# Performance work log

Measured on AMD Instinct MI355X. Metric: run time of the kernel, lower is better.

The kernel has to match this reference:

```python
import jax, jax.numpy as jnp
import numpy as np

B, C_IN, L = 256, 4, 2048
HNODE, GLEN = 256, 24
SIGMA_CONV, SIGMA_NEU = 0.1, 0.1
DROPPROB = 0.5


def setup_inputs() -> dict:
    key = jax.random.key(0)
    ks = jax.random.split(key, 7)
    x = jax.random.normal(ks[0], (B, C_IN, L), dtype=jnp.float32)
    wConv = SIGMA_CONV * jax.random.normal(ks[1], (HNODE, C_IN, GLEN), dtype=jnp.float32)
    wRect = -jax.random.normal(ks[2], (HNODE,), dtype=jnp.float32)
    wHidden = 0.3 * jax.random.normal(ks[3], (2 * HNODE, 2 * HNODE), dtype=jnp.float32)
    wHiddenBias = 0.3 * jax.random.normal(ks[4], (2 * HNODE,), dtype=jnp.float32)
    wNeu = SIGMA_NEU * jax.random.normal(ks[5], (2 * HNODE, 1), dtype=jnp.float32)
    wNeuBias = SIGMA_NEU * jax.random.normal(ks[6], (1,), dtype=jnp.float32)
    return {"x": x, "wConv": wConv, "wRect": wRect, "wHidden": wHidden,
            "wHiddenBias": wHiddenBias, "wNeu": wNeu, "wNeuBias": wNeuBias}


def reference(x, wConv, wRect, wHidden, wHiddenBias, wNeu, wNeuBias):
    # conv1d, stride 1, no padding: [B, HNODE, L-GLEN+1]
    conv = jax.lax.conv_general_dilated(
        x, wConv, window_strides=(1,), padding='VALID',
        dimension_numbers=('NCH', 'OIH', 'NCH'))
    rect = jnp.maximum(conv + wRect[None, :, None], 0.0)  # bias + relu-clamp
    maxPool = jnp.max(rect, axis=2)   # [B, HNODE]
    avgPool = jnp.mean(rect, axis=2)  # [B, HNODE]
    pool = jnp.concatenate([maxPool, avgPool], axis=1)  # [B, 2*HNODE]
    hid = jnp.maximum(pool @ wHidden + wHiddenBias, 0.0)
    out = DROPPROB * (hid @ wNeu) + wNeuBias  # [B, 1]
    return out
```

## Files before the change

kernel.cpp:

```cpp
#include <hip/hip_runtime.h>
#include <stdint.h>

#define CIN   4
#define LEN   2048
#define HN    256
#define GL    24
#define LOUT  2025
#define XPH   1056

typedef short  s16x8 __attribute__((ext_vector_type(8)));
typedef float  f32x4 __attribute__((ext_vector_type(4)));

__device__ float g_part[256][2][512];

static __device__ __forceinline__ uint16_t f2bf(float f) {
    union { float f; uint32_t u; } v; v.f = f;
    uint32_t u = v.u;
    return (uint16_t)((u + 0x7FFFu + ((u >> 16) & 1u)) >> 16);
}

#define MKFRAG(dd, p) \
    ({ uint32_t f0_, f1_, f2_, f3_; \
       if (((p) & 1) == 0) { \
           f0_ = dd[(p)/2];   f1_ = dd[(p)/2+1]; \
           f2_ = dd[(p)/2+2]; f3_ = dd[(p)/2+3]; \
       } else { \
           f0_ = __builtin_amdgcn_alignbit(dd[((p)+1)/2],   dd[((p)-1)/2],   16); \
           f1_ = __builtin_amdgcn_alignbit(dd[((p)+1)/2+1], dd[((p)-1)/2+1], 16); \
           f2_ = __builtin_amdgcn_alignbit(dd[((p)+1)/2+2], dd[((p)-1)/2+2], 16); \
           f3_ = __builtin_amdgcn_alignbit(dd[((p)+1)/2+3], dd[((p)-1)/2+3], 16); \
       } \
       uint4 fu_ = {f0_, f1_, f2_, f3_}; __builtin_bit_cast(s16x8, fu_); })

__global__ __launch_bounds__(1024, 4) void conv_pool_kernel(
    const float* __restrict__ x, const float* __restrict__ wConv,
    const float* __restrict__ wRect)
{
    __shared__ uint16_t xs[CIN * XPH];
    __shared__ float pmax_l[2][HN];
    __shared__ float psum_l[2][HN];

    const int tid  = threadIdx.x;
    const int b    = blockIdx.x >> 1;
    const int wh   = blockIdx.x & 1;
    const int lane = tid & 63;
    const int wid  = tid >> 6;
    const int wp   = wid & 7;
    const int wq   = wid >> 3;
    const int n    = lane & 15;
    const int q    = lane >> 4;

    const float* xb = x + (size_t)b * (CIN * LEN);
    for (int f = tid; f < CIN * (XPH / 4); f += 1024) {
        int c = f / (XPH / 4);
        int k4 = (f - c * (XPH / 4)) * 4;
        int p0 = wh * 1024 + k4;
        uint64_t pk = 0;
        if (p0 < LEN) {
            float4 v = *(const float4*)(xb + c * LEN + p0);
            pk =  (uint64_t)f2bf(v.x)
               | ((uint64_t)f2bf(v.y) << 16)
               | ((uint64_t)f2bf(v.z) << 32)
               | ((uint64_t)f2bf(v.w) << 48);
        }
        *(uint64_t*)&xs[c * XPH + k4] = pk;
    }

    s16x8 bfrag[2][3];
    float negb[2];
    #pragma unroll
    for (int s = 0; s < 2; ++s) {
        int h = wp * 32 + s * 16 + n;
        negb[s] = -wRect[h];
        #pragma unroll
        for (int ks = 0; ks < 3; ++ks) {
            int jb = ks * 4 + q;
            const float* wp_ = wConv + h * (CIN * GL) + jb * 8;
            float4 w0 = *(const float4*)(wp_);
            float4 w1 = *(const float4*)(wp_ + 4);
            s16x8 f;
            f[0]=(short)f2bf(w0.x); f[1]=(short)f2bf(w0.y);
            f[2]=(short)f2bf(w0.z); f[3]=(short)f2bf(w0.w);
            f[4]=(short)f2bf(w1.x); f[5]=(short)f2bf(w1.y);
            f[6]=(short)f2bf(w1.z); f[7]=(short)f2bf(w1.w);
            bfrag[s][ks] = f;
        }
    }

    int abase[3];
    #pragma unroll
    for (int ks = 0; ks < 3; ++ks) {
        int jb = ks * 4 + q;
        int c = jb / 3, g0 = (jb % 3) * 8;
        abase[ks] = c * XPH + g0 + 8 * n;
    }

    __syncthreads();

    float rawmax[2] = {-1e30f, -1e30f};
    float sums[2]   = {0.f, 0.f};
    const f32x4 fzero = {0.f, 0.f, 0.f, 0.f};

    #pragma unroll 1
    for (int tt = 0; tt < 4; ++tt) {
        const int jl = wq * 4 + tt;
        const bool tail = (wh == 1) && (jl == 7);

        uint32_t d0[8], d1[8], d2[8];
        {
            const uint4 r0 = *(const uint4*)&xs[abase[0] + 128 * jl];
            const uint4 r1 = *(const uint4*)&xs[abase[0] + 128 * jl + 8];
            d0[0]=r0.x; d0[1]=r0.y; d0[2]=r0.z; d0[3]=r0.w;
            d0[4]=r1.x; d0[5]=r1.y; d0[6]=r1.z; d0[7]=r1.w;
        }
        {
            const uint4 r0 = *(const uint4*)&xs[abase[1] + 128 * jl];
            const uint4 r1 = *(const uint4*)&xs[abase[1] + 128 * jl + 8];
            d1[0]=r0.x; d1[1]=r0.y; d1[2]=r0.z; d1[3]=r0.w;
            d1[4]=r1.x; d1[5]=r1.y; d1[6]=r1.z; d1[7]=r1.w;
        }
        {
            const uint4 r0 = *(const uint4*)&xs[abase[2] + 128 * jl];
            const uint4 r1 = *(const uint4*)&xs[abase[2] + 128 * jl + 8];
            d2[0]=r0.x; d2[1]=r0.y; d2[2]=r0.z; d2[3]=r0.w;
            d2[4]=r1.x; d2[5]=r1.y; d2[6]=r1.z; d2[7]=r1.w;
        }

        #pragma unroll
        for (int p = 0; p < 8; ++p) {
            s16x8 a0 = MKFRAG(d0, p);
            s16x8 a1 = MKFRAG(d1, p);
            s16x8 a2 = MKFRAG(d2, p);
            f32x4 acc[2];
            acc[0] = __builtin_amdgcn_mfma_f32_16x16x32_bf16(a0, bfrag[0][0], fzero, 0, 0, 0);
            acc[1] = __builtin_amdgcn_mfma_f32_16x16x32_bf16(a0, bfrag[1][0], fzero, 0, 0, 0);
            acc[0] = __builtin_amdgcn_mfma_f32_16x16x32_bf16(a1, bfrag[0][1], acc[0], 0, 0, 0);
            acc[1] = __builtin_amdgcn_mfma_f32_16x16x32_bf16(a1, bfrag[1][1], acc[1], 0, 0, 0);
            acc[0] = __builtin_amdgcn_mfma_f32_16x16x32_bf16(a2, bfrag[0][2], acc[0], 0, 0, 0);
            acc[1] = __builtin_amdgcn_mfma_f32_16x16x32_bf16(a2, bfrag[1][2], acc[1], 0, 0, 0);

            if (!tail) {
                #pragma unroll
                for (int s = 0; s < 2; ++s) {
                    const f32x4 a = acc[s];
                    float t0 = fmaxf(a[0], negb[s]), t1 = fmaxf(a[1], negb[s]);
                    float t2 = fmaxf(a[2], negb[s]), t3 = fmaxf(a[3], negb[s]);
                    sums[s] += (t0 + t1) + (t2 + t3);
                    rawmax[s] = fmaxf(fmaxf(rawmax[s], a[0]), a[1]);
                    rawmax[s] = fmaxf(fmaxf(rawmax[s], a[2]), a[3]);
                }
            } else {
                #pragma unroll
                for (int s = 0; s < 2; ++s) {
                    const f32x4 a = acc[s];
                    #pragma unroll
                    for (int r = 0; r < 4; ++r) {
                        int tpos = p + 128 * 15 + 32 * q + 8 * r;
                        float t = (tpos < LOUT) ? fmaxf(a[r], negb[s])
                                                : negb[s];
                        sums[s]   += t;
                        rawmax[s]  = fmaxf(rawmax[s], t);
                    }
                }
            }
        }
    }

    #pragma unroll
    for (int s = 0; s < 2; ++s) {
        float m  = rawmax[s], sm = sums[s];
        m  = fmaxf(m, __shfl_xor(m, 16, 64));  sm += __shfl_xor(sm, 16, 64);
        m  = fmaxf(m, __shfl_xor(m, 32, 64));  sm += __shfl_xor(sm, 32, 64);
        if (q == 0) {
            int h = wp * 32 + s * 16 + n;
            pmax_l[wq][h] = m;
            psum_l[wq][h] = sm;
        }
    }
    __syncthreads();

    if (tid < HN) {
        g_part[b][wh][tid]       = fmaxf(pmax_l[0][tid], pmax_l[1][tid]);
        g_part[b][wh][256 + tid] = psum_l[0][tid] + psum_l[1][tid];
    }
}

__global__ __launch_bounds__(256, 4) void mlp_kernel(
    const float* __restrict__ wRect, const float* __restrict__ wH,
    const float* __restrict__ bH, const float* __restrict__ wNeu,
    const float* __restrict__ wNeuB, float* __restrict__ out)
{
    __shared__ float pl[8][512];

    const int tid = threadIdx.x;
    const int og  = blockIdx.x & 7;
    const int bg  = blockIdx.x >> 3;
    const int o   = og * 64 + (tid & 63);
    const int wv  = tid >> 6;

    #pragma unroll
    for (int it = 0; it < 4; ++it) {
        int i   = (tid + it * 256) * 4;
        int smp = i >> 9;
        int c   = i & 511;
        const float* p0 = &g_part[bg * 8 + smp][0][c];
        const float* p1 = &g_part[bg * 8 + smp][1][c];
        float4 v0 = *(const float4*)p0;
        float4 v1 = *(const float4*)p1;
        float4 r;
        if (c < 256) {
            float4 wr = *(const float4*)(wRect + c);
            r.x = fmaxf(fmaxf(v0.x, v1.x) + wr.x, 0.f);
            r.y = fmaxf(fmaxf(v0.y, v1.y) + wr.y, 0.f);
            r.z = fmaxf(fmaxf(v0.z, v1.z) + wr.z, 0.f);
            r.w = fmaxf(fmaxf(v0.w, v1.w) + wr.w, 0.f);
        } else {
            float4 wr = *(const float4*)(wRect + c - 256);
            r.x = (v0.x + v1.x + 2048.f * wr.x) * (1.0f / 2025.0f);
            r.y = (v0.y + v1.y + 2048.f * wr.y) * (1.0f / 2025.0f);
            r.z = (v0.z + v1.z + 2048.f * wr.z) * (1.0f / 2025.0f);
            r.w = (v0.w + v1.w + 2048.f * wr.w) * (1.0f / 2025.0f);
        }
        *(float4*)&pl[0][i] = r;
    }
    __syncthreads();

    float acc0 = 0.f, acc1 = 0.f;
    const float* prow0 = &pl[wv * 2][0];
    const float* prow1 = &pl[wv * 2 + 1][0];
    #pragma unroll 4
    for (int i = 0; i < 512; i += 4) {
        float4 p0 = *(const float4*)(prow0 + i);
        float4 p1 = *(const float4*)(prow1 + i);
        float w0 = wH[(i + 0) * 512 + o];
        float w1 = wH[(i + 1) * 512 + o];
        float w2 = wH[(i + 2) * 512 + o];
        float w3 = wH[(i + 3) * 512 + o];
        acc0 = fmaf(p0.x, w0, acc0); acc0 = fmaf(p0.y, w1, acc0);
        acc0 = fmaf(p0.z, w2, acc0); acc0 = fmaf(p0.w, w3, acc0);
        acc1 = fmaf(p1.x, w0, acc1); acc1 = fmaf(p1.y, w1, acc1);
        acc1 = fmaf(p1.z, w2, acc1); acc1 = fmaf(p1.w, w3, acc1);
    }
    float hb  = bH[o];
    float wn  = wNeu[o];
    float v0  = fmaxf(acc0 + hb, 0.f) * wn;
    float v1  = fmaxf(acc1 + hb, 0.f) * wn;
    #pragma unroll
    for (int dlt = 1; dlt < 64; dlt <<= 1) {
        v0 += __shfl_xor(v0, dlt, 64);
        v1 += __shfl_xor(v1, dlt, 64);
    }
    if ((tid & 63) == 0) {
        int b0 = bg * 8 + wv * 2;
        float bias = (og == 0) ? wNeuB[0] : 0.f;
        atomicAdd(&out[b0],     0.5f * v0 + bias);
        atomicAdd(&out[b0 + 1], 0.5f * v1 + bias);
    }
}

extern "C" void kernel_launch(void* const* d_in, const int* in_sizes, int n_in,
                              void* d_out, int out_size, void* d_ws, size_t ws_size,
                              hipStream_t stream) {
    const float* x        = (const float*)d_in[0];
    const float* wConv    = (const float*)d_in[1];
    const float* wRect    = (const float*)d_in[2];
    const float* wHidden  = (const float*)d_in[3];
    const float* wHidBias = (const float*)d_in[4];
    const float* wNeu     = (const float*)d_in[5];
    const float* wNeuBias = (const float*)d_in[6];
    float* out  = (float*)d_out;
    (void)d_ws; (void)ws_size;

    hipMemsetAsync(d_out, 0, 256 * sizeof(float), stream);
    conv_pool_kernel<<<512, 1024, 0, stream>>>(x, wConv, wRect);
    mlp_kernel<<<256, 256, 0, stream>>>(wRect, wHidden, wHidBias, wNeu, wNeuBias, out);
}
```

Measured before the change: 133.3 us.

## Split conv-pool work into quarter-sequence blocks of 512 threads

The conv_pool kernel now uses 1024 blocks of 512 threads, each covering a quarter of the sequence for one sample, where it used 512 blocks of 1024 threads covering halves. Each wave writes its partial max and sum straight to global memory, which removes the shared-memory reduction and the second barrier. The MLP kernel now combines four partials per sample instead of two. This gives smaller blocks that may schedule more evenly, at the cost of more halo loads per block and more partial traffic.

```diff
diff --git a/kernel.cpp b/kernel.cpp
--- a/kernel.cpp
+++ b/kernel.cpp
@@ -6,12 +6,12 @@
 #define HN    256
 #define GL    24
 #define LOUT  2025
-#define XPH   1056
+#define XPQ   544
 
 typedef short  s16x8 __attribute__((ext_vector_type(8)));
 typedef float  f32x4 __attribute__((ext_vector_type(4)));
 
-__device__ float g_part[256][2][512];
+__device__ float g_part[256][4][512];
 
 static __device__ __forceinline__ uint16_t f2bf(float f) {
     union { float f; uint32_t u; } v; v.f = f;
@@ -32,29 +32,25 @@
        } \
        uint4 fu_ = {f0_, f1_, f2_, f3_}; __builtin_bit_cast(s16x8, fu_); })
 
-__global__ __launch_bounds__(1024, 4) void conv_pool_kernel(
+__global__ __launch_bounds__(512, 2) void conv_pool_kernel(
     const float* __restrict__ x, const float* __restrict__ wConv,
     const float* __restrict__ wRect)
 {
-    __shared__ uint16_t xs[CIN * XPH];
-    __shared__ float pmax_l[2][HN];
-    __shared__ float psum_l[2][HN];
+    __shared__ uint16_t xs[CIN * XPQ];
 
     const int tid  = threadIdx.x;
-    const int b    = blockIdx.x >> 1;
-    const int wh   = blockIdx.x & 1;
+    const int b    = blockIdx.x >> 2;
+    const int qt   = blockIdx.x & 3;
     const int lane = tid & 63;
     const int wid  = tid >> 6;
-    const int wp   = wid & 7;
-    const int wq   = wid >> 3;
     const int n    = lane & 15;
     const int q    = lane >> 4;
 
     const float* xb = x + (size_t)b * (CIN * LEN);
-    for (int f = tid; f < CIN * (XPH / 4); f += 1024) {
-        int c = f / (XPH / 4);
-        int k4 = (f - c * (XPH / 4)) * 4;
-        int p0 = wh * 1024 + k4;
+    for (int f = tid; f < CIN * (XPQ / 4); f += 512) {
+        int c  = f / (XPQ / 4);
+        int k4 = (f - c * (XPQ / 4)) * 4;
+        int p0 = qt * 512 + k4;
         uint64_t pk = 0;
         if (p0 < LEN) {
             float4 v = *(const float4*)(xb + c * LEN + p0);
@@ -63,14 +59,14 @@
                | ((uint64_t)f2bf(v.z) << 32)
                | ((uint64_t)f2bf(v.w) << 48);
         }
-        *(uint64_t*)&xs[c * XPH + k4] = pk;
+        *(uint64_t*)&xs[c * XPQ + k4] = pk;
     }
 
     s16x8 bfrag[2][3];
     float negb[2];
     #pragma unroll
     for (int s = 0; s < 2; ++s) {
-        int h = wp * 32 + s * 16 + n;
+        int h = wid * 32 + s * 16 + n;
         negb[s] = -wRect[h];
         #pragma unroll
         for (int ks = 0; ks < 3; ++ks) {
@@ -92,7 +88,7 @@
     for (int ks = 0; ks < 3; ++ks) {
         int jb = ks * 4 + q;
         int c = jb / 3, g0 = (jb % 3) * 8;
-        abase[ks] = c * XPH + g0 + 8 * n;
+        abase[ks] = c * XPQ + g0 + 8 * n;
     }
 
     __syncthreads();
@@ -103,25 +99,24 @@
 
     #pragma unroll 1
     for (int tt = 0; tt < 4; ++tt) {
-        const int jl = wq * 4 + tt;
-        const bool tail = (wh == 1) && (jl == 7);
+        const bool tail = (qt == 3) && (tt == 3);
 
         uint32_t d0[8], d1[8], d2[8];
         {
-            const uint4 r0 = *(const uint4*)&xs[abase[0] + 128 * jl];
-            const uint4 r1 = *(const uint4*)&xs[abase[0] + 128 * jl + 8];
+            const uint4 r0 = *(const uint4*)&xs[abase[0] + 128 * tt];
+            const uint4 r1 = *(const uint4*)&xs[abase[0] + 128 * tt + 8];
             d0[0]=r0.x; d0[1]=r0.y; d0[2]=r0.z; d0[3]=r0.w;
             d0[4]=r1.x; d0[5]=r1.y; d0[6]=r1.z; d0[7]=r1.w;
         }
         {
-            const uint4 r0 = *(const uint4*)&xs[abase[1] + 128 * jl];
-            const uint4 r1 = *(const uint4*)&xs[abase[1] + 128 * jl + 8];
+            const uint4 r0 = *(const uint4*)&xs[abase[1] + 128 * tt];
+            const uint4 r1 = *(const uint4*)&xs[abase[1] + 128 * tt + 8];
             d1[0]=r0.x; d1[1]=r0.y; d1[2]=r0.z; d1[3]=r0.w;
             d1[4]=r1.x; d1[5]=r1.y; d1[6]=r1.z; d1[7]=r1.w;
         }
         {
-            const uint4 r0 = *(const uint4*)&xs[abase[2] + 128 * jl];
-            const uint4 r1 = *(const uint4*)&xs[abase[2] + 128 * jl + 8];
+            const uint4 r0 = *(const uint4*)&xs[abase[2] + 128 * tt];
+            const uint4 r1 = *(const uint4*)&xs[abase[2] + 128 * tt + 8];
             d2[0]=r0.x; d2[1]=r0.y; d2[2]=r0.z; d2[3]=r0.w;
             d2[4]=r1.x; d2[5]=r1.y; d2[6]=r1.z; d2[7]=r1.w;
         }
@@ -172,16 +167,10 @@
         m  = fmaxf(m, __shfl_xor(m, 16, 64));  sm += __shfl_xor(sm, 16, 64);
         m  = fmaxf(m, __shfl_xor(m, 32, 64));  sm += __shfl_xor(sm, 32, 64);
         if (q == 0) {
-            int h = wp * 32 + s * 16 + n;
-            pmax_l[wq][h] = m;
-            psum_l[wq][h] = sm;
-        }
-    }
-    __syncthreads();
-
-    if (tid < HN) {
-        g_part[b][wh][tid]       = fmaxf(pmax_l[0][tid], pmax_l[1][tid]);
-        g_part[b][wh][256 + tid] = psum_l[0][tid] + psum_l[1][tid];
+            int h = wid * 32 + s * 16 + n;
+            g_part[b][qt][h]       = m;
+            g_part[b][qt][256 + h] = sm;
+        }
     }
 }
 
@@ -203,23 +192,24 @@
         int i   = (tid + it * 256) * 4;
         int smp = i >> 9;
         int c   = i & 511;
-        const float* p0 = &g_part[bg * 8 + smp][0][c];
-        const float* p1 = &g_part[bg * 8 + smp][1][c];
-        float4 v0 = *(const float4*)p0;
-        float4 v1 = *(const float4*)p1;
+        const int bb = bg * 8 + smp;
+        float4 v0 = *(const float4*)&g_part[bb][0][c];
+        float4 v1 = *(const float4*)&g_part[bb][1][c];
+        float4 v2 = *(const float4*)&g_part[bb][2][c];
+        float4 v3 = *(const float4*)&g_part[bb][3][c];
         float4 r;
         if (c < 256) {
             float4 wr = *(const float4*)(wRect + c);
-            r.x = fmaxf(fmaxf(v0.x, v1.x) + wr.x, 0.f);
-            r.y = fmaxf(fmaxf(v0.y, v1.y) + wr.y, 0.f);
-            r.z = fmaxf(fmaxf(v0.z, v1.z) + wr.z, 0.f);
-            r.w = fmaxf(fmaxf(v0.w, v1.w) + wr.w, 0.f);
+            r.x = fmaxf(fmaxf(fmaxf(v0.x, v1.x), fmaxf(v2.x, v3.x)) + wr.x, 0.f);
+            r.y = fmaxf(fmaxf(fmaxf(v0.y, v1.y), fmaxf(v2.y, v3.y)) + wr.y, 0.f);
+            r.z = fmaxf(fmaxf(fmaxf(v0.z, v1.z), fmaxf(v2.z, v3.z)) + wr.z, 0.f);
+            r.w = fmaxf(fmaxf(fmaxf(v0.w, v1.w), fmaxf(v2.w, v3.w)) + wr.w, 0.f);
         } else {
             float4 wr = *(const float4*)(wRect + c - 256);
-            r.x = (v0.x + v1.x + 2048.f * wr.x) * (1.0f / 2025.0f);
-            r.y = (v0.y + v1.y + 2048.f * wr.y) * (1.0f / 2025.0f);
-            r.z = (v0.z + v1.z + 2048.f * wr.z) * (1.0f / 2025.0f);
-            r.w = (v0.w + v1.w + 2048.f * wr.w) * (1.0f / 2025.0f);
+            r.x = ((v0.x + v1.x) + (v2.x + v3.x) + 2048.f * wr.x) * (1.0f / 2025.0f);
+            r.y = ((v0.y + v1.y) + (v2.y + v3.y) + 2048.f * wr.y) * (1.0f / 2025.0f);
+            r.z = ((v0.z + v1.z) + (v2.z + v3.z) + 2048.f * wr.z) * (1.0f / 2025.0f);
+            r.w = ((v0.w + v1.w) + (v2.w + v3.w) + 2048.f * wr.w) * (1.0f / 2025.0f);
         }
         *(float4*)&pl[0][i] = r;
     }
@@ -272,6 +262,6 @@
     (void)d_ws; (void)ws_size;
 
     hipMemsetAsync(d_out, 0, 256 * sizeof(float), stream);
-    conv_pool_kernel<<<512, 1024, 0, stream>>>(x, wConv, wRect);
+    conv_pool_kernel<<<1024, 512, 0, stream>>>(x, wConv, wRect);
     mlp_kernel<<<256, 256, 0, stream>>>(wRect, wHidden, wHidBias, wNeu, wNeuBias, out);
 }
```

After: 127.6 us. 4.3% less time.
